# Optimization experiments

Hardware: AMD Instinct MI355X
Metric: run time of the kernel (lower is better)

Reference implementation:

```python
import jax, jax.numpy as jnp
import numpy as np

B, N, K, D = 8, 4096, 16, 256


def layer_norm(x, g, b, eps=1e-5):
    m = jnp.mean(x, axis=-1, keepdims=True)
    v = jnp.var(x, axis=-1, keepdims=True)
    return (x - m) * jax.lax.rsqrt(v + eps) * g + b


def setup_inputs() -> dict:
    key = jax.random.key(0)
    ks = jax.random.split(key, 8)

    def lin(k, fi, fo):
        return (jax.random.normal(k, (fi, fo), jnp.float32) / np.sqrt(fi).astype(np.float32),
                jnp.zeros((fo,), jnp.float32))

    coordinates = jax.random.normal(ks[0], (B, N, 3), jnp.float32)
    W1, b1 = lin(ks[1], 10, D // 4)
    W2, b2 = lin(ks[2], D // 4, D // 2)
    W3, b3 = lin(ks[3], D // 2, D)
    Wa1, ba1 = lin(ks[4], D, D)
    Wa2, ba2 = lin(ks[5], D, D)
    return {
        'coordinates': coordinates,
        'W1': W1, 'b1': b1, 'g1': jnp.ones((D // 4,)), 'be1': jnp.zeros((D // 4,)),
        'W2': W2, 'b2': b2, 'g2': jnp.ones((D // 2,)), 'be2': jnp.zeros((D // 2,)),
        'W3': W3, 'b3': b3, 'g3': jnp.ones((D,)), 'be3': jnp.zeros((D,)),
        'Wa1': Wa1, 'ba1': ba1, 'ga1': jnp.ones((D,)), 'bea1': jnp.zeros((D,)),
        'Wa2': Wa2, 'ba2': ba2,
    }


def reference(coordinates, W1, b1, g1, be1, W2, b2, g2, be2, W3, b3, g3, be3,
              Wa1, ba1, ga1, bea1, Wa2, ba2):
    # kNN via squared-distance matrix (monotone in Euclidean distance)
    sq = jnp.sum(coordinates * coordinates, axis=-1)  # [B,N]
    d2 = sq[:, :, None] + sq[:, None, :] - 2.0 * jnp.einsum('bnd,bmd->bnm', coordinates, coordinates)
    _, idx = jax.lax.top_k(-d2, K)  # smallest K distances, [B,N,K]

    nbr = jax.vmap(lambda c, i: c[i])(coordinates, idx)  # [B,N,K,3]
    rel = nbr - coordinates[:, :, None, :]               # relative positions
    dist = jnp.linalg.norm(rel, axis=-1, keepdims=True)  # [B,N,K,1]
    rn = rel / (dist + 1e-6)
    axy = jnp.arctan2(rn[..., 1], rn[..., 0])[..., None]
    axz = jnp.arctan2(rn[..., 2], rn[..., 0])[..., None]
    ayz = jnp.arctan2(rn[..., 2], rn[..., 1])[..., None]
    geom = jnp.concatenate([dist, rel, axy, axz, ayz, rn], axis=-1)  # [B,N,K,10]

    # encoder MLP
    h = jax.nn.relu(layer_norm(geom @ W1 + b1, g1, be1))
    h = jax.nn.relu(layer_norm(h @ W2 + b2, g2, be2))
    h = layer_norm(h @ W3 + b3, g3, be3)

    agg = jnp.mean(h, axis=2)  # mean over neighbors -> [B,N,D]

    # aggregator MLP
    out = jax.nn.relu(layer_norm(agg @ Wa1 + ba1, ga1, bea1)) @ Wa2 + ba2
    return out
```

## Files before the change

kernel.cpp:

```cpp
#include <hip/hip_runtime.h>
#include <hip/hip_bf16.h>
#include <math.h>

#define BB 8
#define NN 4096
#define KK 16
#define DD 256

typedef __hip_bfloat16 bf16;
typedef _Float16 half8 __attribute__((ext_vector_type(8)));
typedef float f32x4 __attribute__((ext_vector_type(4)));

union HFU { _Float16 h; unsigned short u; };
__device__ __forceinline__ unsigned short f2h(float x) { HFU v; v.h = (_Float16)x; return v.u; }

#define CONV_TOTAL 273344
#define O_COORD 0
#define O_W1 98304
#define O_b1 98944
#define O_g1 99008
#define O_be1 99072
#define O_W2 99136
#define O_b2 107328
#define O_g2 107456
#define O_be2 107584
#define O_W3 107712
#define O_b3 140480
#define O_g3 140736
#define O_be3 140992
#define O_Wa1 141248
#define O_ba1 206784
#define O_ga1 207040
#define O_bea1 207296
#define O_Wa2 207552
#define O_ba2 273088

#define F_W1 0
#define F_W2 2048
#define F_W3 10240
#define F_A1 43008
#define F_A2 108544
#define FRAG_TOTAL 174080

#define PRUNE_MARGIN 0.0625f

struct SrcPtrs {
  const void* p[19];
};

__global__ __launch_bounds__(256) void convert_kernel(SrcPtrs sp, float* __restrict__ dst) {
  static constexpr int OFF[20] = {
      0,      98304,  98944,  99008,  99072,  99136,  107328, 107456, 107584,
      107712, 140480, 140736, 140992, 141248, 206784, 207040, 207296, 207552,
      273088, 273344};
  const int i = blockIdx.x * 256 + threadIdx.x;
  if (i >= CONV_TOTAL) return;
  const unsigned tag = ((const unsigned*)sp.p[3])[0];
  const bool isb = (tag == 0x3F803F80u);
  int s = 0;
#pragma unroll
  for (int j = 1; j < 19; j++)
    if (i >= OFF[j]) s = j;
  const int local = i - OFF[s];
  float v = isb ? __bfloat162float(((const bf16*)sp.p[s])[local])
                : ((const float*)sp.p[s])[local];
  dst[i] = v;
}

__global__ __launch_bounds__(256) void swizzle_kernel(const float* __restrict__ conv,
                                                      unsigned short* __restrict__ frag) {
  const int t = blockIdx.x * 256 + threadIdx.x;
  if (t >= FRAG_TOTAL) return;
  int l, e;
  if (t < 2048) { l = 0; e = t; }
  else if (t < 10240) { l = 1; e = t - 2048; }
  else if (t < 43008) { l = 2; e = t - 10240; }
  else if (t < 108544) { l = 3; e = t - 43008; }
  else { l = 4; e = t - 108544; }
  static constexpr int WOFF[5] = {O_W1, O_W2, O_W3, O_Wa1, O_Wa2};
  static constexpr int NDIM[5] = {64, 128, 256, 256, 256};
  static constexpr int NTC[5] = {4, 8, 16, 16, 16};
  static constexpr int KREAL[5] = {10, 64, 128, 256, 256};
  static constexpr int HOFF[5] = {F_W1, F_W2, F_W3, F_A1, F_A2};
  const int j = e & 7;
  const int lane = (e >> 3) & 63;
  const int tile = e >> 9;
  const int nt = tile % NTC[l];
  const int kt = tile / NTC[l];
  const int k = kt * 32 + (lane >> 4) * 8 + j;
  const int n = nt * 16 + (lane & 15);
  float w = (k < KREAL[l]) ? conv[WOFF[l] + k * NDIM[l] + n] : 0.0f;
  frag[HOFF[l] + e] = f2h(w);
}

__device__ __forceinline__ float sq3_rn(float x, float y, float z) {
  return __fadd_rn(__fadd_rn(__fmul_rn(x, x), __fmul_rn(y, y)), __fmul_rn(z, z));
}
__device__ __forceinline__ float dot3_rn(float ax, float ay, float az, float bx, float by, float bz) {
  return __fadd_rn(__fadd_rn(__fmul_rn(ax, bx), __fmul_rn(ay, by)), __fmul_rn(az, bz));
}
__device__ __forceinline__ unsigned f2ord(float f) {
  unsigned u = __float_as_uint(f);
  return (u & 0x80000000u) ? ~u : (u | 0x80000000u);
}
__device__ __forceinline__ float ord2f(unsigned o) {
  unsigned u = (o & 0x80000000u) ? (o & 0x7FFFFFFFu) : ~o;
  return __uint_as_float(u);
}

__device__ __forceinline__ unsigned long long bitonic64(unsigned long long key, int lane) {
#pragma unroll
  for (int k = 2; k <= 64; k <<= 1) {
#pragma unroll
    for (int jj = k >> 1; jj > 0; jj >>= 1) {
      unsigned long long v = __shfl_xor(key, jj, 64);
      bool asc = ((lane & k) == 0);
      bool up = ((lane & jj) != 0);
      unsigned long long mn = (key < v) ? key : v;
      unsigned long long mx2 = (key < v) ? v : key;
      key = (up == asc) ? mx2 : mn;
    }
  }
  return key;
}

__global__ __launch_bounds__(512) void cellsort_kernel(const float* __restrict__ conv,
                                                       float4* __restrict__ sorted,
                                                       int* __restrict__ sidx) {
  __shared__ unsigned hist[512];
  __shared__ unsigned scanb[512];
  const int b = blockIdx.x;
  const int tid = threadIdx.x;
  const float* cb = conv + O_COORD + (size_t)b * NN * 3;
  hist[tid] = 0;
  __syncthreads();
  float xs[8], ys[8], zs[8];
  int cell[8];
  unsigned rank[8];
#pragma unroll
  for (int u = 0; u < 8; u++) {
    int p = u * 512 + tid;
    float x = cb[p * 3 + 0], y = cb[p * 3 + 1], z = cb[p * 3 + 2];
    xs[u] = x; ys[u] = y; zs[u] = z;
    int ix = min(7, max(0, (int)floorf(x + 4.0f)));
    int iy = min(7, max(0, (int)floorf(y + 4.0f)));
    int iz = min(7, max(0, (int)floorf(z + 4.0f)));
    int m = ((ix & 1) | ((ix & 2) << 2) | ((ix & 4) << 4)) |
            (((iy & 1) | ((iy & 2) << 2) | ((iy & 4) << 4)) << 1) |
            (((iz & 1) | ((iz & 2) << 2) | ((iz & 4) << 4)) << 2);
    cell[u] = m;
    rank[u] = atomicAdd(&hist[m], 1u);
  }
  __syncthreads();
  scanb[tid] = hist[tid];
  __syncthreads();
  for (int off = 1; off < 512; off <<= 1) {
    unsigned t = (tid >= off) ? scanb[tid - off] : 0u;
    __syncthreads();
    scanb[tid] += t;
    __syncthreads();
  }
#pragma unroll
  for (int u = 0; u < 8; u++) {
    unsigned base = scanb[cell[u]] - hist[cell[u]];
    unsigned pos = base + rank[u];
    sorted[(size_t)b * NN + pos] =
        make_float4(xs[u], ys[u], zs[u], sq3_rn(xs[u], ys[u], zs[u]));
    sidx[(size_t)b * NN + pos] = u * 512 + tid;
  }
}

__global__ __launch_bounds__(256) void bbox_kernel(const float4* __restrict__ sorted,
                                                   float4* __restrict__ bbmn,
                                                   float4* __restrict__ bbmx) {
  const int lane = threadIdx.x & 63;
  const int gid = blockIdx.x * 4 + (threadIdx.x >> 6);
  float4 p = sorted[(size_t)gid * 64 + lane];
  float mnx = p.x, mny = p.y, mnz = p.z;
  float mxx = p.x, mxy = p.y, mxz = p.z;
#pragma unroll
  for (int d = 1; d < 64; d <<= 1) {
    mnx = fminf(mnx, __shfl_xor(mnx, d, 64));
    mny = fminf(mny, __shfl_xor(mny, d, 64));
    mnz = fminf(mnz, __shfl_xor(mnz, d, 64));
    mxx = fmaxf(mxx, __shfl_xor(mxx, d, 64));
    mxy = fmaxf(mxy, __shfl_xor(mxy, d, 64));
    mxz = fmaxf(mxz, __shfl_xor(mxz, d, 64));
  }
  if (lane == 0) {
    bbmn[gid] = make_float4(mnx, mny, mnz, 0.0f);
    bbmx[gid] = make_float4(mxx, mxy, mxz, 0.0f);
  }
}

__global__ __launch_bounds__(256) void knn_wave_kernel(const float4* __restrict__ soa,
                                                       const int* __restrict__ sI,
                                                       const float4* __restrict__ bbmn,
                                                       const float4* __restrict__ bbmx,
                                                       int* __restrict__ idx_out) {
  const int lane = threadIdx.x & 63;
  const int wid = blockIdx.x * 4 + (threadIdx.x >> 6);
  const int q0 = wid * 4;
  const int b = q0 >> 12;
  const float4* P = soa + (size_t)b * NN;
  const int* I = sI + (size_t)b * NN;
  const int qr = q0 & (NN - 1);
  const int base = qr >> 6;

  float cx[4], cy[4], cz[4], sqn[4];
  int qix[4];
#pragma unroll
  for (int j = 0; j < 4; j++) {
    float4 c = P[qr + j];
    cx[j] = c.x; cy[j] = c.y; cz[j] = c.z; sqn[j] = c.w;
    qix[j] = I[qr + j];
  }

  float4 bmn = bbmn[b * 64 + lane];
  float4 bmx = bbmx[b * 64 + lane];
  float4 f0 = P[base * 64 + lane];
  int i0 = I[base * 64 + lane];

  float qnx = fminf(fminf(cx[0], cx[1]), fminf(cx[2], cx[3]));
  float qxx = fmaxf(fmaxf(cx[0], cx[1]), fmaxf(cx[2], cx[3]));
  float qny = fminf(fminf(cy[0], cy[1]), fminf(cy[2], cy[3]));
  float qxy = fmaxf(fmaxf(cy[0], cy[1]), fmaxf(cy[2], cy[3]));
  float qnz = fminf(fminf(cz[0], cz[1]), fminf(cz[2], cz[3]));
  float qxz = fmaxf(fmaxf(cz[0], cz[1]), fmaxf(cz[2], cz[3]));

  float dx = fmaxf(fmaxf(bmn.x - qxx, qnx - bmx.x), 0.0f);
  float dy = fmaxf(fmaxf(bmn.y - qxy, qny - bmx.y), 0.0f);
  float dz = fmaxf(fmaxf(bmn.z - qxz, qnz - bmx.z), 0.0f);
  const float lb = dx * dx + dy * dy + dz * dz;

  unsigned long long R[4], pend[4];
  float tauf[4];
  int A[4] = {0, 0, 0, 0};
#pragma unroll
  for (int j = 0; j < 4; j++) pend[j] = ~0ull;

  auto MERGE = [&](int j) {
    unsigned long long key =
        (lane < 16) ? R[j] : ((lane < 16 + A[j]) ? pend[j] : ~0ull);
    key = bitonic64(key, lane);
    R[j] = key;
    tauf[j] = ord2f((unsigned)(unsigned long long)__builtin_amdgcn_readlane(
        (int)(unsigned)(key >> 32), 15));
    A[j] = 0;
  };

  auto APPEND = [&](int j, unsigned long long msk, int cc, unsigned long long key) {
    unsigned rank = __builtin_amdgcn_mbcnt_hi(
        (unsigned)(msk >> 32), __builtin_amdgcn_mbcnt_lo((unsigned)msk, 0u));
    const bool flag = ((msk >> lane) & 1ull) != 0;
    const int lim = 16 + A[j];
    const int nf = lane - (int)rank;
    const int dst = flag ? (lim + (int)rank) : (nf < lim ? nf : nf + cc);
    int src = __builtin_amdgcn_ds_permute(dst << 2, lane) & 63;
    unsigned lo = (unsigned)__builtin_amdgcn_ds_bpermute(src << 2, (int)(unsigned)key);
    unsigned hi = (unsigned)__builtin_amdgcn_ds_bpermute(src << 2, (int)(unsigned)(key >> 32));
    const bool cons = (lane >= lim) && (lane < lim + cc);
    if (cons) pend[j] = (((unsigned long long)hi) << 32) | lo;
    A[j] += cc;
  };

#pragma unroll
  for (int j = 0; j < 4; j++) {
    float dot = dot3_rn(cx[j], cy[j], cz[j], f0.x, f0.y, f0.z);
    float d2 = __fsub_rn(__fadd_rn(sqn[j], f0.w), __fmul_rn(2.0f, dot));
    unsigned long long key =
        (((unsigned long long)f2ord(d2)) << 32) | (unsigned)i0;
    key = bitonic64(key, lane);
    R[j] = key;
    tauf[j] = ord2f((unsigned)(unsigned long long)__builtin_amdgcn_readlane(
        (int)(unsigned)(key >> 32), 15));
  }

  float tmax = fmaxf(fmaxf(tauf[0], tauf[1]), fmaxf(tauf[2], tauf[3]));
  unsigned long long mask =
      __ballot(lb <= tmax + PRUNE_MARGIN) & ~(1ull << base);
  const int ro = (base + 1) & 63;
  auto rot = [&](unsigned long long m) {
    return ro ? ((m >> ro) | (m << (64 - ro))) : m;
  };
  unsigned long long rm = rot(mask);

  int tA = -1, tB = -1, iA = 0, iB = 0;
  float4 fA, fB;
  if (rm) {
    int tz = __builtin_ctzll(rm); rm &= rm - 1;
    tA = (ro + tz) & 63; fA = P[tA * 64 + lane]; iA = I[tA * 64 + lane];
  }
  if (rm) {
    int tz = __builtin_ctzll(rm); rm &= rm - 1;
    tB = (ro + tz) & 63; fB = P[tB * 64 + lane]; iB = I[tB * 64 + lane];
  }
  while (tA >= 0) {
    const float4 c = fA;
    const int iv = iA;
    tA = tB; fA = fB; iA = iB;
    if (rm) {
      int tz = __builtin_ctzll(rm); rm &= rm - 1;
      tB = (ro + tz) & 63; fB = P[tB * 64 + lane]; iB = I[tB * 64 + lane];
    } else {
      tB = -1;
    }
    float d2v[4];
    unsigned long long pm[4];
#pragma unroll
    for (int j = 0; j < 4; j++) {
      float dot = dot3_rn(cx[j], cy[j], cz[j], c.x, c.y, c.z);
      d2v[j] = __fsub_rn(__fadd_rn(sqn[j], c.w), __fmul_rn(2.0f, dot));
      pm[j] = __ballot(d2v[j] <= tauf[j]);
    }
    if (!(pm[0] | pm[1] | pm[2] | pm[3])) continue;
#pragma unroll
    for (int j = 0; j < 4; j++) {
      unsigned long long rem = pm[j];
      if (!rem) continue;
      const unsigned long long key =
          (((unsigned long long)f2ord(d2v[j])) << 32) | (unsigned)iv;
      int cc = __builtin_popcountll(rem);
      while (A[j] + cc > 48) {
        if (A[j] == 0) {
          unsigned long long take = rem & 0xFFFFFFFFull;
          APPEND(j, take, __builtin_popcountll(take), key);
          rem ^= take;
        }
        MERGE(j);
        rem &= __ballot(d2v[j] <= tauf[j]);
        cc = __builtin_popcountll(rem);
      }
      if (cc) APPEND(j, rem, cc, key);
    }
    tmax = fmaxf(fmaxf(tauf[0], tauf[1]), fmaxf(tauf[2], tauf[3]));
    rm &= rot(__ballot(lb <= tmax + PRUNE_MARGIN));
  }

#pragma unroll
  for (int j = 0; j < 4; j++) {
    if (A[j]) MERGE(j);
    if (lane < KK)
      idx_out[((size_t)b * NN + (unsigned)qix[j]) * KK + lane] =
          (int)(R[j] & 0xFFFFFFFFull);
  }
}

template <int KT>
__device__ __forceinline__ void load_afrags(half8* A, const unsigned short* lF,
                                            int rowe, int lane) {
#pragma unroll
  for (int kt = 0; kt < KT; kt++) {
    int off = (lane & 15) * rowe + kt * 32 + (lane >> 4) * 8;
    A[kt] = *reinterpret_cast<const half8*>(lF + off);
  }
}

template <int NT>
__device__ __forceinline__ void init_acc(f32x4* acc, const float* __restrict__ bias,
                                         int lane) {
  const int col = lane & 15;
#pragma unroll
  for (int nt = 0; nt < NT; nt++) {
    float bv = bias[nt * 16 + col];
    acc[nt] = {bv, bv, bv, bv};
  }
}

template <int KT, int NT>
__device__ __forceinline__ void gemm_acc(f32x4* acc, const half8* A,
                                         const unsigned short* bb, int lane) {
#pragma unroll
  for (int kt = 0; kt < KT; kt++)
#pragma unroll
    for (int nt = 0; nt < NT; nt++) {
      const half8 bf = *reinterpret_cast<const half8*>(bb + (kt * NT + nt) * 512 + lane * 8);
      acc[nt] = __builtin_amdgcn_mfma_f32_16x16x32_f16(A[kt], bf, acc[nt], 0, 0, 0);
    }
}

template <int NT>
__device__ __forceinline__ void ln_stats(const f32x4* acc, float* m, float* rs) {
  float s[4] = {0.f, 0.f, 0.f, 0.f}, s2[4] = {0.f, 0.f, 0.f, 0.f};
#pragma unroll
  for (int nt = 0; nt < NT; nt++)
#pragma unroll
    for (int r = 0; r < 4; r++) {
      float v = acc[nt][r];
      s[r] += v;
      s2[r] += v * v;
    }
#pragma unroll
  for (int msk = 1; msk <= 8; msk <<= 1)
#pragma unroll
    for (int r = 0; r < 4; r++) {
      s[r] += __shfl_xor(s[r], msk, 64);
      s2[r] += __shfl_xor(s2[r], msk, 64);
    }
  const float invN = 1.0f / (NT * 16);
#pragma unroll
  for (int r = 0; r < 4; r++) {
    m[r] = s[r] * invN;
    float var = s2[r] * invN - m[r] * m[r];
    rs[r] = rsqrtf(var + 1e-5f);
  }
}

template <int NT, bool RELU>
__device__ __forceinline__ void ln_store(const f32x4* acc, const float* m, const float* rs,
                                         const float* __restrict__ g, const float* __restrict__ be,
                                         unsigned short* lF, int rowe, int lane) {
  const int col = lane & 15;
  const int rbase = (lane >> 4) * 4;
#pragma unroll
  for (int nt = 0; nt < NT; nt++) {
    float gv = g[nt * 16 + col], bv = be[nt * 16 + col];
#pragma unroll
    for (int r = 0; r < 4; r++) {
      float v = (acc[nt][r] - m[r]) * rs[r] * gv + bv;
      if (RELU) v = fmaxf(v, 0.0f);
      lF[(rbase + r) * rowe + nt * 16 + col] = f2h(v);
    }
  }
}

__device__ __forceinline__ void stage_b(unsigned short* bbuf,
                                        const unsigned short* __restrict__ src,
                                        int n_u4, int tid) {
  const uint4* s = reinterpret_cast<const uint4*>(src);
  uint4* d = reinterpret_cast<uint4*>(bbuf);
  for (int i = tid; i < n_u4; i += 256) d[i] = s[i];
}

#define ROWE_E 136
#define PSTR_E (16 * ROWE_E)

__global__ __launch_bounds__(256, 3) void encoder_mfma(
    const float* __restrict__ conv, const int* __restrict__ nbr,
    const unsigned short* __restrict__ frag, unsigned short* __restrict__ agF) {
  __shared__ unsigned short planes[4 * PSTR_E];
  __shared__ unsigned short Bbuf[10240];
  const int tid = threadIdx.x;
  const int lane = tid & 63;
  const int wave = tid >> 6;
  const int point = blockIdx.x * 4 + wave;
  const int b = point >> 12;
  const int n = point & (NN - 1);
  const float* cb = conv + O_COORD + (size_t)b * NN * 3;
  unsigned short* lF = planes + wave * PSTR_E;
  const int g = lane >> 4;
  const int col = lane & 15;

  {
    int pl = tid >> 6, row = (tid >> 2) & 15, part = tid & 3;
    *reinterpret_cast<uint4*>(planes + pl * PSTR_E + row * ROWE_E + part * 8) =
        make_uint4(0u, 0u, 0u, 0u);
    stage_b(Bbuf, frag + F_W1, 1280, tid);
  }
  __syncthreads();

  if (lane < 16) {
    float cxq = cb[n * 3 + 0], cyq = cb[n * 3 + 1], czq = cb[n * 3 + 2];
    int id = nbr[(size_t)point * KK + lane];
    float rx = __fsub_rn(cb[id * 3 + 0], cxq);
    float ry = __fsub_rn(cb[id * 3 + 1], cyq);
    float rz = __fsub_rn(cb[id * 3 + 2], czq);
    float dist = __fsqrt_rn(sq3_rn(rx, ry, rz));
    float den = __fadd_rn(dist, 1e-6f);
    float ux = __fdiv_rn(rx, den), uy = __fdiv_rn(ry, den), uz = __fdiv_rn(rz, den);
    float ge[10];
    ge[0] = dist; ge[1] = rx; ge[2] = ry; ge[3] = rz;
    ge[4] = atan2f(uy, ux); ge[5] = atan2f(uz, ux); ge[6] = atan2f(uz, uy);
    ge[7] = ux; ge[8] = uy; ge[9] = uz;
#pragma unroll
    for (int c = 0; c < 10; c++) lF[lane * ROWE_E + c] = f2h(ge[c]);
  }

  {
    half8 x0;
    load_afrags<1>(&x0, lF, ROWE_E, lane);
    f32x4 a1[4];
#pragma unroll
    for (int m = 0; m < 4; m++) {
      const float4 bv = *reinterpret_cast<const float4*>(conv + O_b1 + m * 16 + g * 4);
      a1[m] = {bv.x, bv.y, bv.z, bv.w};
      const half8 wf = *reinterpret_cast<const half8*>(Bbuf + m * 512 + lane * 8);
      a1[m] = __builtin_amdgcn_mfma_f32_16x16x32_f16(wf, x0, a1[m], 0, 0, 0);
    }
    float s = 0.f, s2 = 0.f;
#pragma unroll
    for (int m = 0; m < 4; m++)
#pragma unroll
      for (int r = 0; r < 4; r++) { float v = a1[m][r]; s += v; s2 += v * v; }
    s += __shfl_xor(s, 16, 64); s += __shfl_xor(s, 32, 64);
    s2 += __shfl_xor(s2, 16, 64); s2 += __shfl_xor(s2, 32, 64);
    const float mu = s * (1.0f / 64.0f);
    const float rsg = rsqrtf(s2 * (1.0f / 64.0f) - mu * mu + 1e-5f);
#pragma unroll
    for (int m = 0; m < 4; m++) {
      const float4 gv = *reinterpret_cast<const float4*>(conv + O_g1 + m * 16 + g * 4);
      const float4 bev = *reinterpret_cast<const float4*>(conv + O_be1 + m * 16 + g * 4);
      unsigned long long pk = 0;
#pragma unroll
      for (int r = 0; r < 4; r++) {
        float v = fmaxf((a1[m][r] - mu) * rsg * (&gv.x)[r] + (&bev.x)[r], 0.0f);
        pk |= ((unsigned long long)f2h(v)) << (16 * r);
      }
      *reinterpret_cast<unsigned long long*>(lF + col * ROWE_E + m * 16 + g * 4) = pk;
    }
  }

  {
    half8 x2[2];
    load_afrags<2>(x2, lF, ROWE_E, lane);
    f32x4 a2[8];
#pragma unroll
    for (int m = 0; m < 8; m++) {
      const float4 bv = *reinterpret_cast<const float4*>(conv + O_b2 + m * 16 + g * 4);
      a2[m] = {bv.x, bv.y, bv.z, bv.w};
    }
#pragma unroll
    for (int kt = 0; kt < 2; kt++)
#pragma unroll
      for (int m = 0; m < 8; m++) {
        const half8 wf =
            *reinterpret_cast<const half8*>(Bbuf + 2048 + (kt * 8 + m) * 512 + lane * 8);
        a2[m] = __builtin_amdgcn_mfma_f32_16x16x32_f16(wf, x2[kt], a2[m], 0, 0, 0);
      }
    float s = 0.f, s2 = 0.f;
#pragma unroll
    for (int m = 0; m < 8; m++)
#pragma unroll
      for (int r = 0; r < 4; r++) { float v = a2[m][r]; s += v; s2 += v * v; }
    s += __shfl_xor(s, 16, 64); s += __shfl_xor(s, 32, 64);
    s2 += __shfl_xor(s2, 16, 64); s2 += __shfl_xor(s2, 32, 64);
    const float mu = s * (1.0f / 128.0f);
    const float rsg = rsqrtf(s2 * (1.0f / 128.0f) - mu * mu + 1e-5f);
#pragma unroll
    for (int m = 0; m < 8; m++) {
      const float4 gv = *reinterpret_cast<const float4*>(conv + O_g2 + m * 16 + g * 4);
      const float4 bev = *reinterpret_cast<const float4*>(conv + O_be2 + m * 16 + g * 4);
      unsigned long long pk = 0;
#pragma unroll
      for (int r = 0; r < 4; r++) {
        float v = fmaxf((a2[m][r] - mu) * rsg * (&gv.x)[r] + (&bev.x)[r], 0.0f);
        pk |= ((unsigned long long)f2h(v)) << (16 * r);
      }
      *reinterpret_cast<unsigned long long*>(lF + col * ROWE_E + m * 16 + g * 4) = pk;
    }
  }

  half8 A3[4];
  load_afrags<4>(A3, lF, ROWE_E, lane);
  f32x4 acc[16];
  init_acc<16>(acc, conv + O_b3, lane);
  {
    const unsigned short* W3 = frag + F_W3;
#pragma unroll
    for (int kt = 0; kt < 4; kt++)
#pragma unroll
      for (int nt = 0; nt < 16; nt++) {
        const half8 bf =
            *reinterpret_cast<const half8*>(W3 + (kt * 16 + nt) * 512 + lane * 8);
        acc[nt] = __builtin_amdgcn_mfma_f32_16x16x32_f16(A3[kt], bf, acc[nt], 0, 0, 0);
      }
  }

  {
    float m[4], rs[4];
    ln_stats<16>(acc, m, rs);
    float sv[16];
#pragma unroll
    for (int nt = 0; nt < 16; nt++) {
      float gvv = conv[O_g3 + nt * 16 + col], bvv = conv[O_be3 + nt * 16 + col];
      float s = 0.f;
#pragma unroll
      for (int r = 0; r < 4; r++) s += (acc[nt][r] - m[r]) * rs[r] * gvv + bvv;
      s += __shfl_xor(s, 16, 64);
      s += __shfl_xor(s, 32, 64);
      sv[nt] = s * (1.0f / 16.0f);
    }
    if (lane < 16) {
      size_t base = (size_t)point * DD;
#pragma unroll
      for (int nt = 0; nt < 16; nt++) agF[base + nt * 16 + lane] = f2h(sv[nt]);
    }
  }
}

#define ROWE_A 264

__global__ __launch_bounds__(256) void aggmlp_mfma(
    const float* __restrict__ conv, const unsigned short* __restrict__ agF,
    const unsigned short* __restrict__ a1, const unsigned short* __restrict__ a2,
    const unsigned* __restrict__ g1raw, void* __restrict__ out) {
  __shared__ unsigned short lds[4][16 * ROWE_A];
  const int lane = threadIdx.x & 63;
  const int wave = threadIdx.x >> 6;
  const int row0 = (blockIdx.x * 4 + wave) * 16;
  unsigned short* lF = lds[wave];

#pragma unroll
  for (int t = 0; t < 8; t++) {
    int v = t * 64 + lane;
    int row = v >> 5;
    int c0 = (v & 31) * 8;
    *reinterpret_cast<uint4*>(lF + row * ROWE_A + c0) =
        *reinterpret_cast<const uint4*>(agF + ((size_t)(row0 + row) * DD + c0));
  }
  __syncthreads();

  float m[4], rs[4];
  f32x4 acc[16];
  {
    half8 A[8];
    load_afrags<8>(A, lF, ROWE_A, lane);
    init_acc<16>(acc, conv + O_ba1, lane);
    gemm_acc<8, 16>(acc, A, a1, lane);
    ln_stats<16>(acc, m, rs);
    ln_store<16, true>(acc, m, rs, conv + O_ga1, conv + O_bea1, lF, ROWE_A, lane);
  }
  __syncthreads();
  {
    half8 A[8];
    load_afrags<8>(A, lF, ROWE_A, lane);
    init_acc<16>(acc, conv + O_ba2, lane);
    gemm_acc<8, 16>(acc, A, a2, lane);
  }
  const bool isb = (g1raw[0] == 0x3F803F80u);
  const int col = lane & 15;
  const int rbase = (lane >> 4) * 4;
  if (isb) {
    bf16* o = (bf16*)out;
#pragma unroll
    for (int nt = 0; nt < 16; nt++)
#pragma unroll
      for (int r = 0; r < 4; r++)
        o[(size_t)(row0 + rbase + r) * DD + nt * 16 + col] = __float2bfloat16(acc[nt][r]);
  } else {
    float* o = (float*)out;
#pragma unroll
    for (int nt = 0; nt < 16; nt++)
#pragma unroll
      for (int r = 0; r < 4; r++)
        o[(size_t)(row0 + rbase + r) * DD + nt * 16 + col] = acc[nt][r];
  }
}

extern "C" void kernel_launch(void* const* d_in, const int* in_sizes, int n_in,
                              void* d_out, int out_size, void* d_ws, size_t ws_size,
                              hipStream_t stream) {
  char* ws = (char*)d_ws;
  float* conv = (float*)ws;
  int* idx_ws = (int*)(ws + 1093376);
  unsigned short* agF = (unsigned short*)(ws + 3190528);
  unsigned short* frag = (unsigned short*)(ws + 19967744);
  float4* sorted = (float4*)(ws + 20315904);
  int* sidx = (int*)(ws + 20840192);
  float4* bbmn = (float4*)(ws + 20971264);
  float4* bbmx = (float4*)(ws + 20979456);

  SrcPtrs sp;
  for (int i = 0; i < 19; i++) sp.p[i] = d_in[i];

  convert_kernel<<<(CONV_TOTAL + 255) / 256, 256, 0, stream>>>(sp, conv);
  swizzle_kernel<<<(FRAG_TOTAL + 255) / 256, 256, 0, stream>>>(conv, frag);
  cellsort_kernel<<<BB, 512, 0, stream>>>(conv, sorted, sidx);
  bbox_kernel<<<BB * 64 / 4, 256, 0, stream>>>(sorted, bbmn, bbmx);

  knn_wave_kernel<<<BB * NN / 16, 256, 0, stream>>>(sorted, sidx, bbmn, bbmx, idx_ws);

  encoder_mfma<<<BB * NN / 4, 256, 0, stream>>>(conv, idx_ws, frag, agF);

  aggmlp_mfma<<<BB * NN / 64, 256, 0, stream>>>(conv, agF, frag + F_A1, frag + F_A2,
                                                (const unsigned*)d_in[3], d_out);
}
```

Before: 375.7 us.

## Split aggregator MLP output columns across two waves per row tile

The aggregator kernel now runs 512 threads per block, and each 16-row tile is handled by two waves that each compute half of the 256 output columns. LayerNorm statistics are combined across the wave pair through a shared-memory reduction with an extra barrier. This halves the accumulator registers per wave and doubles the wave count, aiming at more latency hiding in the final MLP. The cost is the extra synchronisation, and each wave still loads the full A fragments.

```diff
diff --git a/kernel.cpp b/kernel.cpp
--- a/kernel.cpp
+++ b/kernel.cpp
@@ -406,24 +406,6 @@
   }
 }
 
-template <int NT, bool RELU>
-__device__ __forceinline__ void ln_store(const f32x4* acc, const float* m, const float* rs,
-                                         const float* __restrict__ g, const float* __restrict__ be,
-                                         unsigned short* lF, int rowe, int lane) {
-  const int col = lane & 15;
-  const int rbase = (lane >> 4) * 4;
-#pragma unroll
-  for (int nt = 0; nt < NT; nt++) {
-    float gv = g[nt * 16 + col], bv = be[nt * 16 + col];
-#pragma unroll
-    for (int r = 0; r < 4; r++) {
-      float v = (acc[nt][r] - m[r]) * rs[r] * gv + bv;
-      if (RELU) v = fmaxf(v, 0.0f);
-      lF[(rbase + r) * rowe + nt * 16 + col] = f2h(v);
-    }
-  }
-}
-
 __device__ __forceinline__ void stage_b(unsigned short* bbuf,
                                         const unsigned short* __restrict__ src,
                                         int n_u4, int tid) {
@@ -590,60 +572,124 @@
 
 #define ROWE_A 264
 
-__global__ __launch_bounds__(256) void aggmlp_mfma(
+__global__ __launch_bounds__(512) void aggmlp_mfma(
     const float* __restrict__ conv, const unsigned short* __restrict__ agF,
     const unsigned short* __restrict__ a1, const unsigned short* __restrict__ a2,
     const unsigned* __restrict__ g1raw, void* __restrict__ out) {
   __shared__ unsigned short lds[4][16 * ROWE_A];
-  const int lane = threadIdx.x & 63;
-  const int wave = threadIdx.x >> 6;
-  const int row0 = (blockIdx.x * 4 + wave) * 16;
-  unsigned short* lF = lds[wave];
-
-#pragma unroll
-  for (int t = 0; t < 8; t++) {
-    int v = t * 64 + lane;
+  __shared__ float sred[8][64][8];
+  const int tid = threadIdx.x;
+  const int lane = tid & 63;
+  const int wave = tid >> 6;
+  const int p = wave >> 1;
+  const int nh = wave & 1;
+  const int row0 = blockIdx.x * 64;
+  unsigned short* lF = lds[p];
+  const int col = lane & 15;
+  const int rbase = (lane >> 4) * 4;
+
+#pragma unroll
+  for (int t = 0; t < 4; t++) {
+    int v = t * 512 + tid;
     int row = v >> 5;
     int c0 = (v & 31) * 8;
-    *reinterpret_cast<uint4*>(lF + row * ROWE_A + c0) =
+    *reinterpret_cast<uint4*>(&lds[row >> 4][(row & 15) * ROWE_A + c0]) =
         *reinterpret_cast<const uint4*>(agF + ((size_t)(row0 + row) * DD + c0));
   }
   __syncthreads();
 
+  half8 A[8];
+  load_afrags<8>(A, lF, ROWE_A, lane);
+
+  f32x4 acc[8];
+#pragma unroll
+  for (int n = 0; n < 8; n++) {
+    float bv = conv[O_ba1 + (nh * 8 + n) * 16 + col];
+    acc[n] = {bv, bv, bv, bv};
+  }
+#pragma unroll
+  for (int kt = 0; kt < 8; kt++)
+#pragma unroll
+    for (int n = 0; n < 8; n++) {
+      const half8 bf = *reinterpret_cast<const half8*>(
+          a1 + (kt * 16 + nh * 8 + n) * 512 + lane * 8);
+      acc[n] = __builtin_amdgcn_mfma_f32_16x16x32_f16(A[kt], bf, acc[n], 0, 0, 0);
+    }
+  float s[4] = {0.f, 0.f, 0.f, 0.f}, s2[4] = {0.f, 0.f, 0.f, 0.f};
+#pragma unroll
+  for (int n = 0; n < 8; n++)
+#pragma unroll
+    for (int r = 0; r < 4; r++) {
+      float v = acc[n][r];
+      s[r] += v;
+      s2[r] += v * v;
+    }
+#pragma unroll
+  for (int msk = 1; msk <= 8; msk <<= 1)
+#pragma unroll
+    for (int r = 0; r < 4; r++) {
+      s[r] += __shfl_xor(s[r], msk, 64);
+      s2[r] += __shfl_xor(s2[r], msk, 64);
+    }
+#pragma unroll
+  for (int r = 0; r < 4; r++) {
+    sred[wave][lane][r] = s[r];
+    sred[wave][lane][4 + r] = s2[r];
+  }
+  __syncthreads();
   float m[4], rs[4];
-  f32x4 acc[16];
-  {
-    half8 A[8];
-    load_afrags<8>(A, lF, ROWE_A, lane);
-    init_acc<16>(acc, conv + O_ba1, lane);
-    gemm_acc<8, 16>(acc, A, a1, lane);
-    ln_stats<16>(acc, m, rs);
-    ln_store<16, true>(acc, m, rs, conv + O_ga1, conv + O_bea1, lF, ROWE_A, lane);
+#pragma unroll
+  for (int r = 0; r < 4; r++) {
+    s[r] += sred[wave ^ 1][lane][r];
+    s2[r] += sred[wave ^ 1][lane][4 + r];
+    m[r] = s[r] * (1.0f / 256.0f);
+    float var = s2[r] * (1.0f / 256.0f) - m[r] * m[r];
+    rs[r] = rsqrtf(var + 1e-5f);
+  }
+#pragma unroll
+  for (int n = 0; n < 8; n++) {
+    const int nt = nh * 8 + n;
+    float gv = conv[O_ga1 + nt * 16 + col], bv = conv[O_bea1 + nt * 16 + col];
+#pragma unroll
+    for (int r = 0; r < 4; r++) {
+      float v = fmaxf((acc[n][r] - m[r]) * rs[r] * gv + bv, 0.0f);
+      lF[(rbase + r) * ROWE_A + nt * 16 + col] = f2h(v);
+    }
   }
   __syncthreads();
-  {
-    half8 A[8];
-    load_afrags<8>(A, lF, ROWE_A, lane);
-    init_acc<16>(acc, conv + O_ba2, lane);
-    gemm_acc<8, 16>(acc, A, a2, lane);
-  }
+
+  load_afrags<8>(A, lF, ROWE_A, lane);
+#pragma unroll
+  for (int n = 0; n < 8; n++) {
+    float bv = conv[O_ba2 + (nh * 8 + n) * 16 + col];
+    acc[n] = {bv, bv, bv, bv};
+  }
+#pragma unroll
+  for (int kt = 0; kt < 8; kt++)
+#pragma unroll
+    for (int n = 0; n < 8; n++) {
+      const half8 bf = *reinterpret_cast<const half8*>(
+          a2 + (kt * 16 + nh * 8 + n) * 512 + lane * 8);
+      acc[n] = __builtin_amdgcn_mfma_f32_16x16x32_f16(A[kt], bf, acc[n], 0, 0, 0);
+    }
+
   const bool isb = (g1raw[0] == 0x3F803F80u);
-  const int col = lane & 15;
-  const int rbase = (lane >> 4) * 4;
+  const int orow = row0 + p * 16 + rbase;
   if (isb) {
     bf16* o = (bf16*)out;
 #pragma unroll
-    for (int nt = 0; nt < 16; nt++)
+    for (int n = 0; n < 8; n++)
 #pragma unroll
       for (int r = 0; r < 4; r++)
-        o[(size_t)(row0 + rbase + r) * DD + nt * 16 + col] = __float2bfloat16(acc[nt][r]);
+        o[(size_t)(orow + r) * DD + (nh * 8 + n) * 16 + col] =
+            __float2bfloat16(acc[n][r]);
   } else {
     float* o = (float*)out;
 #pragma unroll
-    for (int nt = 0; nt < 16; nt++)
+    for (int n = 0; n < 8; n++)
 #pragma unroll
       for (int r = 0; r < 4; r++)
-        o[(size_t)(row0 + rbase + r) * DD + nt * 16 + col] = acc[nt][r];
+        o[(size_t)(orow + r) * DD + (nh * 8 + n) * 16 + col] = acc[n][r];
   }
 }
 
@@ -672,6 +718,6 @@
 
   encoder_mfma<<<BB * NN / 4, 256, 0, stream>>>(conv, idx_ws, frag, agF);
 
-  aggmlp_mfma<<<BB * NN / 64, 256, 0, stream>>>(conv, agF, frag + F_A1, frag + F_A2,
+  aggmlp_mfma<<<BB * NN / 64, 512, 0, stream>>>(conv, agF, frag + F_A1, frag + F_A2,
                                                 (const unsigned*)d_in[3], d_out);
 }
```

Measured after the change: 380.0 us. No clear change (+1.2%).
